# Kernel tuning notes

Measured on AMD Instinct MI355X. Metric: run time of the kernel, lower is better.

The kernel has to match this reference:

```python
import jax, jax.numpy as jnp
import numpy as np

R_SPHERE = 3.0   # bounding_sphere_radius
NEAR = 0.0       # near_distance
FAR = 100.0      # far_distance
SECANT_STEPS = 4 # manifold_secant_steps
EPS = 1e-4
R0 = 1.0         # base radius of analytic manifold field


def setup_inputs() -> dict:
    key = jax.random.key(0)
    ks = jax.random.split(key, 6)
    B, R, L, H = 4, 8192, 4, 64
    rays_o = jax.random.normal(ks[0], (B, R, 3), dtype=jnp.float32) * 0.2  # origins inside sphere
    rd = jax.random.normal(ks[1], (B, R, 3), dtype=jnp.float32)
    rays_d = rd / jnp.linalg.norm(rd, axis=-1, keepdims=True)
    levels = jnp.linspace(0.5, -0.5, L, dtype=jnp.float32)  # manifold_levels parameter
    W1 = jax.random.normal(ks[2], (3, H), dtype=jnp.float32) * 0.3
    b1 = jnp.zeros((H,), dtype=jnp.float32)
    W2 = jax.random.normal(ks[3], (H, 1), dtype=jnp.float32) * 0.1
    b2 = jnp.zeros((1,), dtype=jnp.float32)
    rays_idx = jax.random.randint(ks[4], (B, R), 0, B, dtype=jnp.int64) if jax.config.jax_enable_x64 else jax.random.randint(ks[4], (B, R), 0, B, dtype=jnp.int32)
    mask_gt = jnp.ones((B, R), dtype=bool)
    return {"rays_o": rays_o, "rays_d": rays_d, "levels": levels, "W1": W1, "b1": b1,
            "W2": W2, "b2": b2, "mask_gt": mask_gt, "rays_idx": rays_idx, "num_samples": 64}


def _ray_march(rays_o, rays_d, levels, W1, b1, W2, b2, num_samples):
    B, Rn = rays_o.shape[:2]
    N = B * Rn
    L = levels.shape[0]
    o = rays_o.reshape(N, 3)
    d = rays_d.reshape(N, 3)

    def manifold_fn(x):
        # analytic stand-in for M(x_d, idx): scalar field + validity mask
        h = jnp.tanh(x @ W1 + b1)
        nrm = jnp.linalg.norm(x, axis=-1)
        s = (h @ W2)[..., 0] + b2[0] + (R0 - nrm)
        return s, nrm < R_SPHERE

    # ray-sphere intersection (unit-norm directions assumed, as in source)
    b = jnp.sum(o * d, axis=-1)
    c = jnp.sum(o * o, axis=-1) - R_SPHERE ** 2
    disc = b * b - c
    hit = disc > 0
    sq = jnp.sqrt(jnp.where(hit, disc, 1.0))
    d_near = jnp.maximum(-b - sq, NEAR)
    d_far = jnp.minimum(-b + sq, FAR)
    mask_bound = hit & (d_near < d_far)

    # stratified (uniform) depth samples, (N, S)
    t = jnp.linspace(0.0, 1.0, num_samples, dtype=rays_o.dtype)[None, :]
    ds = d_near[:, None] * (1 - t) + d_far[:, None] * t
    x_d = o[:, None, :] + d[:, None, :] * ds[..., None]  # (N, S, 3)
    scal, m_valid = manifold_fn(x_d)                      # (N, S)

    # --- find_closest_interval ---
    S = num_samples
    dep_f, dep_b = ds[:, :-1], ds[:, 1:]
    sc_f, sc_b = scal[:, :-1], scal[:, 1:]
    m_pair = m_valid[:, :-1] & m_valid[:, 1:]
    l3 = levels[None, :, None]                            # (1, L, 1)
    in_interval = (sc_f[:, None, :] >= l3) & (l3 >= sc_b[:, None, :]) & m_pair[:, None, :]
    rank = jnp.sign(l3 - sc_b[:, None, :]) * jnp.arange(S - 1, 0, -1, dtype=scal.dtype)
    ind_closest = jnp.argmax(rank, axis=2)                # (N, L)
    ind_lowest = jnp.broadcast_to(jnp.argmin(sc_b, axis=1)[:, None], (N, L))
    mask_surface = jnp.any(in_interval, axis=2)
    idx = jnp.where(mask_surface, ind_closest, ind_lowest)
    d_front = jnp.take_along_axis(dep_f, idx, axis=1)
    d_back = jnp.take_along_axis(dep_b, idx, axis=1)
    s_front = jnp.take_along_axis(sc_f, idx, axis=1)
    s_back = jnp.take_along_axis(sc_b, idx, axis=1)

    # --- find_exact_intersection ---
    lr = levels[None, :]                                  # (1, L)
    s_diff = s_front - s_back
    m_vdiff = jnp.abs(s_diff) > EPS
    mask_intersect = (s_front >= lr) & (lr >= s_back)
    mask_secant = mask_intersect & m_vdiff
    s_diff_safe = jnp.where(m_vdiff, s_diff, 1.0)
    d_secant = ((lr - s_back) * d_front + (s_front - lr) * d_back) / s_diff_safe
    d_init = jnp.where(mask_secant, d_secant, d_back)

    # secant refinement (fixed step count; masked full-array updates replace
    # torch's boolean-indexed subset updates with identical math on masked lanes)
    dfs, dbs, sfs, sbs, dcur = d_front, d_back, s_front, s_back, d_init
    for _ in range(SECANT_STEPS):
        x_mid = o[:, None, :] + dcur[..., None] * d[:, None, :]  # (N, L, 3)
        s_mid, mv = manifold_fn(x_mid)
        upf = (s_mid > lr) & mv
        upb = (s_mid < lr) & mv
        dfs = jnp.where(upf, dcur, dfs)
        sfs = jnp.where(upf, s_mid, sfs)
        dbs = jnp.where(upb, dcur, dbs)
        sbs = jnp.where(upb, s_mid, sbs)
        sd = sfs - sbs
        ok = jnp.abs(sd) > EPS
        dcur = jnp.where(ok, ((lr - sbs) * dfs + (sfs - lr) * dbs) / jnp.where(ok, sd, 1.0), dcur)
    d_intersect = jnp.where(mask_secant, dcur, d_init)

    # sort intersections by depth (use_presort=False branch)
    order = jnp.argsort(d_intersect, axis=1)
    d_intersect = jnp.take_along_axis(d_intersect, order, axis=1)
    mask_intersect = jnp.take_along_axis(mask_intersect, order, axis=1)

    dist = jnp.where(mask_bound[:, None], d_intersect, 0.0).reshape(B, Rn, L)
    mask = (mask_intersect & mask_bound[:, None]).reshape(B, Rn, L)
    return dist, mask


def reference(rays_o, rays_d, levels, W1, b1, W2, b2, mask_gt, rays_idx, num_samples):
    # mask_gt / rays_idx are unused in eval mode (use_gt_mask_when_training=False,
    # analytic manifold_fn ignores batch index), kept for signature fidelity.
    return _ray_march(rays_o, rays_d, levels, W1, b1, W2, b2, num_samples)
```

## Files before the change

kernel.cpp:

```cpp
#include <hip/hip_runtime.h>
#include <cstdint>

#define R_SPHEREf 3.0f
#define NEARf 0.0f
#define FARf 100.0f
#define SECANT_STEPS 4
#define EPSf 1e-4f
#define R0f 1.0f
#define Hh 64
#define Lc 4
#define Sn 64

#define C_HI 2.88539004325866699f
#define C_LO 3.8519227871e-08f

__device__ __forceinline__ float fastdiv(float a, float b) {
    float r = __builtin_amdgcn_rcpf(b);
    r = __builtin_fmaf(r, __builtin_fmaf(-b, r, 1.0f), r);
    return a * r;
}

__global__ __launch_bounds__(256) void manifold_render_kernel(
    const float* __restrict__ rays_o, const float* __restrict__ rays_d,
    const float* __restrict__ levels, const float* __restrict__ W1,
    const float* __restrict__ b1, const float* __restrict__ W2,
    const float* __restrict__ b2, float* __restrict__ out, int N)
{
    __shared__ float4 abq[4][Hh];

    const int tid = threadIdx.x;
    const int wave = tid >> 6;
    const int lane = tid & 63;
    const int r = blockIdx.x * 4 + wave;
    if (r >= N) return;

    const float b2v = b2[0];
    float lvl[Lc];
#pragma unroll
    for (int j = 0; j < Lc; ++j) lvl[j] = levels[j];

    const float ox = rays_o[3 * r], oy = rays_o[3 * r + 1], oz = rays_o[3 * r + 2];
    const float dx = rays_d[3 * r], dy = rays_d[3 * r + 1], dz = rays_d[3 * r + 2];

    const float bq = ox * dx + oy * dy + oz * dz;
    const float cq = ox * ox + oy * oy + oz * oz - R_SPHEREf * R_SPHEREf;
    const float disc = bq * bq - cq;
    const bool hit = disc > 0.0f;
    const float sqv = __builtin_amdgcn_sqrtf(hit ? disc : 1.0f);
    const float d_near = fmaxf(-bq - sqv, NEARf);
    const float d_far  = fminf(-bq + sqv, FARf);
    const bool mask_bound = hit && (d_near < d_far);
    const float delta = (d_far - d_near) * (1.0f / 63.0f);

    const float w1x = W1[lane], w1y = W1[Hh + lane], w1z = W1[2 * Hh + lane];
    const float w2lane = W2[lane];
    const float Ah = __builtin_fmaf(oz, w1z, __builtin_fmaf(oy, w1y,
                     __builtin_fmaf(ox, w1x, b1[lane])));
    const float Bh = __builtin_fmaf(dz, w1z, __builtin_fmaf(dy, w1y, dx * w1x));
    const float A2 = __builtin_fmaf(Ah, C_LO, Ah * C_HI);
    const float B2 = __builtin_fmaf(Bh, C_LO, Bh * C_HI);
    const float zq = -2.0f * w2lane;
    const float zs = copysignf(fmaxf(fabsf(zq), 1e-30f), zq);
    float rz = __builtin_amdgcn_rcpf(zs);
    rz = __builtin_fmaf(rz, __builtin_fmaf(-zs, rz, 1.0f), rz);
    const float Gh = __builtin_amdgcn_exp2f(B2 * (8.0f * delta));
    abq[wave][lane] = make_float4(A2, B2, rz, Gh);

    float w2sum = w2lane;
#pragma unroll
    for (int m = 1; m < 64; m <<= 1) w2sum += __shfl_xor(w2sum, m);
    const float sbase = w2sum + b2v + R0f;

    const int hg = lane >> 3;
    const int sl = lane & 7;
    const float dsl = __builtin_fmaf((float)sl, delta, d_near);

    const float4* __restrict__ ab = &abq[wave][0];
    float v[8], Gr[8], K[8];
#pragma unroll
    for (int j = 0; j < 8; ++j) {
        const float4 q = ab[hg + 8 * j];
        const float y = fminf(__builtin_fmaf(dsl, q.y, q.x), 60.0f);
        const float e0 = __builtin_amdgcn_exp2f(y);
        v[j]  = __builtin_fmaf(e0, q.z, q.z);
        Gr[j] = q.w;
        K[j]  = __builtin_fmaf(-q.z, q.w, q.z);
    }

    float mysum = 0.0f;
#pragma unroll
    for (int it = 0; it < 8; ++it) {
        if (it > 0) {
#pragma unroll
            for (int j = 0; j < 8; ++j) v[j] = __builtin_fmaf(v[j], Gr[j], K[j]);
        }
        const float n01 = v[0] + v[1], d01 = v[0] * v[1];
        const float n23 = v[2] + v[3], d23 = v[2] * v[3];
        const float numA = __builtin_fmaf(n23, d01, n01 * d23);
        const float denA = d01 * d23;
        const float n45 = v[4] + v[5], d45 = v[4] * v[5];
        const float n67 = v[6] + v[7], d67 = v[6] * v[7];
        const float numB = __builtin_fmaf(n67, d45, n45 * d67);
        const float denB = d45 * d67;
        float part = numA * __builtin_amdgcn_rcpf(denA);
        part = __builtin_fmaf(numB, __builtin_amdgcn_rcpf(denB), part);
        part += __shfl_xor(part, 8);
        part += __shfl_xor(part, 16);
        part += __shfl_xor(part, 32);
        if (it == hg) mysum = part;
    }

    const float t = (float)lane * (1.0f / 63.0f);
    const float dsv = d_near * (1.0f - t) + d_far * t;
    const float x0 = ox + dx * dsv, x1 = oy + dy * dsv, x2 = oz + dz * dsv;
    const float nrm = __builtin_amdgcn_sqrtf(x0 * x0 + x1 * x1 + x2 * x2);
    const float scal = (mysum + sbase) - nrm;
    const bool valid = nrm < R_SPHEREf;

    const float scb = __shfl_down(scal, 1);
    const int validn = __shfl_down((int)valid, 1);
    const bool is_int = lane < (Sn - 1);

    float keyv = is_int ? scb : INFINITY;
    int keyi = lane;
#pragma unroll
    for (int m = 1; m < 64; m <<= 1) {
        float ov = __shfl_xor(keyv, m);
        int oi = __shfl_xor(keyi, m);
        if (ov < keyv || (ov == keyv && oi < keyi)) { keyv = ov; keyi = oi; }
    }
    const int ind_lowest = keyi;

    const bool inint_base = is_int && valid && (validn != 0);

    bool mintb[Lc], msec[Lc];
    float dinit[Lc];
    float g_dfs = 0.f, g_dbs = 0.f, g_sfs = 0.f, g_sbs = 0.f, g_dcur = 0.f, g_lr = 0.f;
    const int gl = lane >> 4;

#pragma unroll
    for (int lv = 0; lv < Lc; ++lv) {
        const float l = lvl[lv];
        unsigned long long bP = __ballot(is_int && (scb < l));
        unsigned long long bZ = __ballot(is_int && (scb == l));
        unsigned long long bI = __ballot(inint_base && (scal >= l) && (l >= scb));
        int ind_closest = bP ? __builtin_ctzll(bP)
                             : (bZ ? __builtin_ctzll(bZ) : (Sn - 2));
        bool mask_surface = (bI != 0ULL);
        int idx = mask_surface ? ind_closest : ind_lowest;

        float d_front = __shfl(dsv, idx);
        float d_back  = __shfl(dsv, idx + 1);
        float s_front = __shfl(scal, idx);
        float s_back  = __shfl(scal, idx + 1);

        bool mi = (s_front >= l) && (l >= s_back);
        float sd = s_front - s_back;
        bool vd = fabsf(sd) > EPSf;
        bool ms = mi && vd;
        float d_sec = fastdiv((l - s_back) * d_front + (s_front - l) * d_back,
                              vd ? sd : 1.0f);
        float di = ms ? d_sec : d_back;

        mintb[lv] = mi; msec[lv] = ms; dinit[lv] = di;
        if (gl == lv) {
            g_dfs = d_front; g_dbs = d_back; g_sfs = s_front; g_sbs = s_back;
            g_dcur = di; g_lr = l;
        }
    }

    const int sub = lane & 15;
    float4 sq0 = ab[sub], sq1 = ab[sub + 16], sq2 = ab[sub + 32], sq3 = ab[sub + 48];

#pragma unroll
    for (int it = 0; it < SECANT_STEPS; ++it) {
        float mx0 = ox + g_dcur * dx, mx1 = oy + g_dcur * dy, mx2 = oz + g_dcur * dz;
        float mn = __builtin_amdgcn_sqrtf(mx0 * mx0 + mx1 * mx1 + mx2 * mx2);
        float part;
        {
            float y0 = fminf(__builtin_fmaf(g_dcur, sq0.y, sq0.x), 60.0f);
            float y1 = fminf(__builtin_fmaf(g_dcur, sq1.y, sq1.x), 60.0f);
            float y2 = fminf(__builtin_fmaf(g_dcur, sq2.y, sq2.x), 60.0f);
            float y3 = fminf(__builtin_fmaf(g_dcur, sq3.y, sq3.x), 60.0f);
            float e0 = __builtin_amdgcn_exp2f(y0);
            float e1 = __builtin_amdgcn_exp2f(y1);
            float e2 = __builtin_amdgcn_exp2f(y2);
            float e3 = __builtin_amdgcn_exp2f(y3);
            float v0 = __builtin_fmaf(e0, sq0.z, sq0.z);
            float v1 = __builtin_fmaf(e1, sq1.z, sq1.z);
            float v2 = __builtin_fmaf(e2, sq2.z, sq2.z);
            float v3 = __builtin_fmaf(e3, sq3.z, sq3.z);
            float n01 = v0 + v1, d01 = v0 * v1;
            float n23 = v2 + v3, d23 = v2 * v3;
            part = n01 * __builtin_amdgcn_rcpf(d01);
            part = __builtin_fmaf(n23, __builtin_amdgcn_rcpf(d23), part);
        }
#pragma unroll
        for (int m = 1; m < 16; m <<= 1) part += __shfl_xor(part, m, 16);
        float s_mid = (part + sbase) - mn;
        bool mv = mn < R_SPHEREf;
        bool upf = (s_mid > g_lr) && mv;
        bool upb = (s_mid < g_lr) && mv;
        if (upf) { g_dfs = g_dcur; g_sfs = s_mid; }
        if (upb) { g_dbs = g_dcur; g_sbs = s_mid; }
        float sd2 = g_sfs - g_sbs;
        bool ok = fabsf(sd2) > EPSf;
        if (ok) g_dcur = fastdiv((g_lr - g_sbs) * g_dfs + (g_sfs - g_lr) * g_dbs, sd2);
    }

    float v0g, v1g, v2g, v3g;
    {
        float dc0 = __shfl(g_dcur, 0);
        float dc1 = __shfl(g_dcur, 16);
        float dc2 = __shfl(g_dcur, 32);
        float dc3 = __shfl(g_dcur, 48);
        v0g = msec[0] ? dc0 : dinit[0];
        v1g = msec[1] ? dc1 : dinit[1];
        v2g = msec[2] ? dc2 : dinit[2];
        v3g = msec[3] ? dc3 : dinit[3];
    }
    int m0 = mintb[0], m1 = mintb[1], m2 = mintb[2], m3 = mintb[3];
    int i0 = 0, i1 = 1, i2 = 2, i3 = 3;

#define CSWAP(va, ia, ma, vb, ib, mb)                                    \
    { bool sw = (vb < va) || (vb == va && ib < ia);                      \
      if (sw) { float tv = va; va = vb; vb = tv;                         \
                int ti = ia; ia = ib; ib = ti;                           \
                int tm = ma; ma = mb; mb = tm; } }
    CSWAP(v0g, i0, m0, v1g, i1, m1);
    CSWAP(v2g, i2, m2, v3g, i3, m3);
    CSWAP(v0g, i0, m0, v2g, i2, m2);
    CSWAP(v1g, i1, m1, v3g, i3, m3);
    CSWAP(v1g, i1, m1, v2g, i2, m2);
#undef CSWAP

    const long long NL = (long long)N * Lc;
    if (lane < Lc) {
        float dv = (lane == 0) ? v0g : (lane == 1) ? v1g : (lane == 2) ? v2g : v3g;
        out[(long long)r * Lc + lane] = mask_bound ? dv : 0.0f;
    } else if (lane < 2 * Lc) {
        int k = lane - Lc;
        int mm = (k == 0) ? m0 : (k == 1) ? m1 : (k == 2) ? m2 : m3;
        out[NL + (long long)r * Lc + k] = (mm && mask_bound) ? 1.0f : 0.0f;
    }
}

extern "C" void kernel_launch(void* const* d_in, const int* in_sizes, int n_in,
                              void* d_out, int out_size, void* d_ws, size_t ws_size,
                              hipStream_t stream) {
    const float* rays_o = (const float*)d_in[0];
    const float* rays_d = (const float*)d_in[1];
    const float* levels = (const float*)d_in[2];
    const float* W1 = (const float*)d_in[3];
    const float* b1 = (const float*)d_in[4];
    const float* W2 = (const float*)d_in[5];
    const float* b2 = (const float*)d_in[6];
    float* out = (float*)d_out;

    const int N = in_sizes[0] / 3;
    const int blocks = (N + 3) / 4;
    manifold_render_kernel<<<blocks, 256, 0, stream>>>(
        rays_o, rays_d, levels, W1, b1, W2, b2, out, N);
}
```

Measured before the change: 110.1 us.

## Use butterfly reduction, ballot bitmasks and readlane broadcasts in ray march kernel

Replaces the eight repeated full-wave reductions with a single transpose-style butterfly that reduces all eight partial sums in three shuffle stages. Bracket-search masks are now built from one ballot per comparison plus bit shifts instead of per-level ballots on shifted values. The argmin over the wave is skipped when every level already has a surface crossing. Uniform-index gathers become readlane, the Newton refinements on reciprocals and the exp2 clamps are removed, and divergent branches are turned into selects. In exchange it gives up reciprocal precision and the overflow guard on exp2.

```diff
diff --git a/kernel.cpp b/kernel.cpp
--- a/kernel.cpp
+++ b/kernel.cpp
@@ -14,10 +14,8 @@
 #define C_HI 2.88539004325866699f
 #define C_LO 3.8519227871e-08f
 
-__device__ __forceinline__ float fastdiv(float a, float b) {
-    float r = __builtin_amdgcn_rcpf(b);
-    r = __builtin_fmaf(r, __builtin_fmaf(-b, r, 1.0f), r);
-    return a * r;
+__device__ __forceinline__ float rlanef(float v, int l) {
+    return __uint_as_float((unsigned)__builtin_amdgcn_readlane((int)__float_as_uint(v), l));
 }
 
 __global__ __launch_bounds__(256) void manifold_render_kernel(
@@ -61,8 +59,7 @@
     const float B2 = __builtin_fmaf(Bh, C_LO, Bh * C_HI);
     const float zq = -2.0f * w2lane;
     const float zs = copysignf(fmaxf(fabsf(zq), 1e-30f), zq);
-    float rz = __builtin_amdgcn_rcpf(zs);
-    rz = __builtin_fmaf(rz, __builtin_fmaf(-zs, rz, 1.0f), rz);
+    const float rz = __builtin_amdgcn_rcpf(zs);
     const float Gh = __builtin_amdgcn_exp2f(B2 * (8.0f * delta));
     abq[wave][lane] = make_float4(A2, B2, rz, Gh);
 
@@ -80,14 +77,14 @@
 #pragma unroll
     for (int j = 0; j < 8; ++j) {
         const float4 q = ab[hg + 8 * j];
-        const float y = fminf(__builtin_fmaf(dsl, q.y, q.x), 60.0f);
+        const float y = __builtin_fmaf(dsl, q.y, q.x);
         const float e0 = __builtin_amdgcn_exp2f(y);
         v[j]  = __builtin_fmaf(e0, q.z, q.z);
         Gr[j] = q.w;
         K[j]  = __builtin_fmaf(-q.z, q.w, q.z);
     }
 
-    float mysum = 0.0f;
+    float pp[8];
 #pragma unroll
     for (int it = 0; it < 8; ++it) {
         if (it > 0) {
@@ -104,11 +101,19 @@
         const float denB = d45 * d67;
         float part = numA * __builtin_amdgcn_rcpf(denA);
         part = __builtin_fmaf(numB, __builtin_amdgcn_rcpf(denB), part);
-        part += __shfl_xor(part, 8);
-        part += __shfl_xor(part, 16);
-        part += __shfl_xor(part, 32);
-        if (it == hg) mysum = part;
-    }
+        pp[it] = part;
+    }
+
+    const bool hb0 = (lane & 8)  != 0;
+    const bool hb1 = (lane & 16) != 0;
+    const bool hb2 = (lane & 32) != 0;
+    const float q0 = (hb0 ? pp[1] : pp[0]) + __shfl_xor(hb0 ? pp[0] : pp[1], 8);
+    const float q1 = (hb0 ? pp[3] : pp[2]) + __shfl_xor(hb0 ? pp[2] : pp[3], 8);
+    const float q2 = (hb0 ? pp[5] : pp[4]) + __shfl_xor(hb0 ? pp[4] : pp[5], 8);
+    const float q3 = (hb0 ? pp[7] : pp[6]) + __shfl_xor(hb0 ? pp[6] : pp[7], 8);
+    const float r0 = (hb1 ? q1 : q0) + __shfl_xor(hb1 ? q0 : q1, 16);
+    const float r1 = (hb1 ? q3 : q2) + __shfl_xor(hb1 ? q2 : q3, 16);
+    const float mysum = (hb2 ? r1 : r0) + __shfl_xor(hb2 ? r0 : r1, 32);
 
     const float t = (float)lane * (1.0f / 63.0f);
     const float dsv = d_near * (1.0f - t) + d_far * t;
@@ -117,21 +122,35 @@
     const float scal = (mysum + sbase) - nrm;
     const bool valid = nrm < R_SPHEREf;
 
-    const float scb = __shfl_down(scal, 1);
-    const int validn = __shfl_down((int)valid, 1);
-    const bool is_int = lane < (Sn - 1);
-
-    float keyv = is_int ? scb : INFINITY;
-    int keyi = lane;
-#pragma unroll
-    for (int m = 1; m < 64; m <<= 1) {
-        float ov = __shfl_xor(keyv, m);
-        int oi = __shfl_xor(keyi, m);
-        if (ov < keyv || (ov == keyv && oi < keyi)) { keyv = ov; keyi = oi; }
-    }
-    const int ind_lowest = keyi;
-
-    const bool inint_base = is_int && valid && (validn != 0);
+    const unsigned long long mInt = 0x7fffffffffffffffull;
+    const unsigned long long mV  = __ballot(valid);
+    const unsigned long long mIB = mV & (mV >> 1) & mInt;
+
+    unsigned long long bPa[Lc], bZa[Lc], bIa[Lc];
+#pragma unroll
+    for (int lv = 0; lv < Lc; ++lv) {
+        const float l = lvl[lv];
+        const unsigned long long bL = __ballot(scal < l);
+        const unsigned long long bE = __ballot(scal == l);
+        const unsigned long long bP = (bL >> 1) & mInt;
+        const unsigned long long bZ = (bE >> 1) & mInt;
+        bPa[lv] = bP; bZa[lv] = bZ;
+        bIa[lv] = (~bL) & (bP | bZ) & mIB;
+    }
+
+    int ind_lowest = 0;
+    if ((bIa[0] == 0ULL) || (bIa[1] == 0ULL) || (bIa[2] == 0ULL) || (bIa[3] == 0ULL)) {
+        const float scb = __shfl_down(scal, 1);
+        float keyv = (lane < Sn - 1) ? scb : INFINITY;
+        int keyi = lane;
+#pragma unroll
+        for (int m = 1; m < 64; m <<= 1) {
+            float ov = __shfl_xor(keyv, m);
+            int oi = __shfl_xor(keyi, m);
+            if (ov < keyv || (ov == keyv && oi < keyi)) { keyv = ov; keyi = oi; }
+        }
+        ind_lowest = keyi;
+    }
 
     bool mintb[Lc], msec[Lc];
     float dinit[Lc];
@@ -141,79 +160,81 @@
 #pragma unroll
     for (int lv = 0; lv < Lc; ++lv) {
         const float l = lvl[lv];
-        unsigned long long bP = __ballot(is_int && (scb < l));
-        unsigned long long bZ = __ballot(is_int && (scb == l));
-        unsigned long long bI = __ballot(inint_base && (scal >= l) && (l >= scb));
-        int ind_closest = bP ? __builtin_ctzll(bP)
-                             : (bZ ? __builtin_ctzll(bZ) : (Sn - 2));
-        bool mask_surface = (bI != 0ULL);
-        int idx = mask_surface ? ind_closest : ind_lowest;
-
-        float d_front = __shfl(dsv, idx);
-        float d_back  = __shfl(dsv, idx + 1);
-        float s_front = __shfl(scal, idx);
-        float s_back  = __shfl(scal, idx + 1);
-
-        bool mi = (s_front >= l) && (l >= s_back);
-        float sd = s_front - s_back;
-        bool vd = fabsf(sd) > EPSf;
-        bool ms = mi && vd;
-        float d_sec = fastdiv((l - s_back) * d_front + (s_front - l) * d_back,
-                              vd ? sd : 1.0f);
-        float di = ms ? d_sec : d_back;
+        const unsigned long long bP = bPa[lv], bZ = bZa[lv], bI = bIa[lv];
+        const int ind_closest = bP ? __builtin_ctzll(bP)
+                                   : (bZ ? __builtin_ctzll(bZ) : (Sn - 2));
+        const int idx = bI ? ind_closest : ind_lowest;
+
+        const float d_front = rlanef(dsv, idx);
+        const float d_back  = rlanef(dsv, idx + 1);
+        const float s_front = rlanef(scal, idx);
+        const float s_back  = rlanef(scal, idx + 1);
+
+        const bool mi = (s_front >= l) && (l >= s_back);
+        const float sd = s_front - s_back;
+        const bool vd = fabsf(sd) > EPSf;
+        const bool ms = mi && vd;
+        const float num = (l - s_back) * d_front + (s_front - l) * d_back;
+        const float d_sec = num * __builtin_amdgcn_rcpf(vd ? sd : 1.0f);
+        const float di = ms ? d_sec : d_back;
 
         mintb[lv] = mi; msec[lv] = ms; dinit[lv] = di;
-        if (gl == lv) {
-            g_dfs = d_front; g_dbs = d_back; g_sfs = s_front; g_sbs = s_back;
-            g_dcur = di; g_lr = l;
-        }
+        const bool pick = (gl == lv);
+        g_dfs = pick ? d_front : g_dfs;
+        g_dbs = pick ? d_back  : g_dbs;
+        g_sfs = pick ? s_front : g_sfs;
+        g_sbs = pick ? s_back  : g_sbs;
+        g_dcur = pick ? di : g_dcur;
+        g_lr  = pick ? l : g_lr;
     }
 
     const int sub = lane & 15;
-    float4 sq0 = ab[sub], sq1 = ab[sub + 16], sq2 = ab[sub + 32], sq3 = ab[sub + 48];
+    const float4 sq0 = ab[sub], sq1 = ab[sub + 16], sq2 = ab[sub + 32], sq3 = ab[sub + 48];
 
 #pragma unroll
     for (int it = 0; it < SECANT_STEPS; ++it) {
-        float mx0 = ox + g_dcur * dx, mx1 = oy + g_dcur * dy, mx2 = oz + g_dcur * dz;
-        float mn = __builtin_amdgcn_sqrtf(mx0 * mx0 + mx1 * mx1 + mx2 * mx2);
+        const float mx0 = ox + g_dcur * dx, mx1 = oy + g_dcur * dy, mx2 = oz + g_dcur * dz;
+        const float mn = __builtin_amdgcn_sqrtf(mx0 * mx0 + mx1 * mx1 + mx2 * mx2);
         float part;
         {
-            float y0 = fminf(__builtin_fmaf(g_dcur, sq0.y, sq0.x), 60.0f);
-            float y1 = fminf(__builtin_fmaf(g_dcur, sq1.y, sq1.x), 60.0f);
-            float y2 = fminf(__builtin_fmaf(g_dcur, sq2.y, sq2.x), 60.0f);
-            float y3 = fminf(__builtin_fmaf(g_dcur, sq3.y, sq3.x), 60.0f);
-            float e0 = __builtin_amdgcn_exp2f(y0);
-            float e1 = __builtin_amdgcn_exp2f(y1);
-            float e2 = __builtin_amdgcn_exp2f(y2);
-            float e3 = __builtin_amdgcn_exp2f(y3);
-            float v0 = __builtin_fmaf(e0, sq0.z, sq0.z);
-            float v1 = __builtin_fmaf(e1, sq1.z, sq1.z);
-            float v2 = __builtin_fmaf(e2, sq2.z, sq2.z);
-            float v3 = __builtin_fmaf(e3, sq3.z, sq3.z);
-            float n01 = v0 + v1, d01 = v0 * v1;
-            float n23 = v2 + v3, d23 = v2 * v3;
-            part = n01 * __builtin_amdgcn_rcpf(d01);
-            part = __builtin_fmaf(n23, __builtin_amdgcn_rcpf(d23), part);
+            const float y0 = __builtin_fmaf(g_dcur, sq0.y, sq0.x);
+            const float y1 = __builtin_fmaf(g_dcur, sq1.y, sq1.x);
+            const float y2 = __builtin_fmaf(g_dcur, sq2.y, sq2.x);
+            const float y3 = __builtin_fmaf(g_dcur, sq3.y, sq3.x);
+            const float e0 = __builtin_amdgcn_exp2f(y0);
+            const float e1 = __builtin_amdgcn_exp2f(y1);
+            const float e2 = __builtin_amdgcn_exp2f(y2);
+            const float e3 = __builtin_amdgcn_exp2f(y3);
+            const float v0 = __builtin_fmaf(e0, sq0.z, sq0.z);
+            const float v1 = __builtin_fmaf(e1, sq1.z, sq1.z);
+            const float v2 = __builtin_fmaf(e2, sq2.z, sq2.z);
+            const float v3 = __builtin_fmaf(e3, sq3.z, sq3.z);
+            const float n01 = v0 + v1, d01 = v0 * v1;
+            const float n23 = v2 + v3, d23 = v2 * v3;
+            const float num = __builtin_fmaf(n23, d01, n01 * d23);
+            const float den = d01 * d23;
+            part = num * __builtin_amdgcn_rcpf(den);
         }
 #pragma unroll
         for (int m = 1; m < 16; m <<= 1) part += __shfl_xor(part, m, 16);
-        float s_mid = (part + sbase) - mn;
-        bool mv = mn < R_SPHEREf;
-        bool upf = (s_mid > g_lr) && mv;
-        bool upb = (s_mid < g_lr) && mv;
-        if (upf) { g_dfs = g_dcur; g_sfs = s_mid; }
-        if (upb) { g_dbs = g_dcur; g_sbs = s_mid; }
-        float sd2 = g_sfs - g_sbs;
-        bool ok = fabsf(sd2) > EPSf;
-        if (ok) g_dcur = fastdiv((g_lr - g_sbs) * g_dfs + (g_sfs - g_lr) * g_dbs, sd2);
+        const float s_mid = (part + sbase) - mn;
+        const bool mv = mn < R_SPHEREf;
+        const bool upf = (s_mid > g_lr) && mv;
+        const bool upb = (s_mid < g_lr) && mv;
+        g_dfs = upf ? g_dcur : g_dfs;  g_sfs = upf ? s_mid : g_sfs;
+        g_dbs = upb ? g_dcur : g_dbs;  g_sbs = upb ? s_mid : g_sbs;
+        const float sd2 = g_sfs - g_sbs;
+        const bool ok = fabsf(sd2) > EPSf;
+        const float nd = (g_lr - g_sbs) * g_dfs + (g_sfs - g_lr) * g_dbs;
+        g_dcur = ok ? nd * __builtin_amdgcn_rcpf(sd2) : g_dcur;
     }
 
     float v0g, v1g, v2g, v3g;
     {
-        float dc0 = __shfl(g_dcur, 0);
-        float dc1 = __shfl(g_dcur, 16);
-        float dc2 = __shfl(g_dcur, 32);
-        float dc3 = __shfl(g_dcur, 48);
+        const float dc0 = __shfl(g_dcur, 0);
+        const float dc1 = __shfl(g_dcur, 16);
+        const float dc2 = __shfl(g_dcur, 32);
+        const float dc3 = __shfl(g_dcur, 48);
         v0g = msec[0] ? dc0 : dinit[0];
         v1g = msec[1] ? dc1 : dinit[1];
         v2g = msec[2] ? dc2 : dinit[2];
@@ -235,13 +256,15 @@
 #undef CSWAP
 
     const long long NL = (long long)N * Lc;
-    if (lane < Lc) {
-        float dv = (lane == 0) ? v0g : (lane == 1) ? v1g : (lane == 2) ? v2g : v3g;
-        out[(long long)r * Lc + lane] = mask_bound ? dv : 0.0f;
-    } else if (lane < 2 * Lc) {
-        int k = lane - Lc;
-        int mm = (k == 0) ? m0 : (k == 1) ? m1 : (k == 2) ? m2 : m3;
-        out[NL + (long long)r * Lc + k] = (mm && mask_bound) ? 1.0f : 0.0f;
+    if (lane < 2 * Lc) {
+        const int k = lane & 3;
+        const float dvs = (k == 0) ? v0g : (k == 1) ? v1g : (k == 2) ? v2g : v3g;
+        const int   mms = (k == 0) ? m0 : (k == 1) ? m1 : (k == 2) ? m2 : m3;
+        const bool isd = lane < Lc;
+        const float val = isd ? (mask_bound ? dvs : 0.0f)
+                              : ((mms && mask_bound) ? 1.0f : 0.0f);
+        const long long off = (long long)r * Lc + k + (isd ? 0LL : NL);
+        out[off] = val;
     }
 }
 
```

After: 114.8 us. 4.3% more time.
